# Performance work log

Hardware: AMD Instinct MI355X
Metric: run time of the kernel (lower is better)

## Reference

```python
import jax, jax.numpy as jnp
import numpy as np

jax.config.update("jax_enable_x64", True)  # int64 keys for lattice hashing

_EPS = float(np.finfo(np.float64).eps)
_SIGMA_SPATIAL = 5.0   # spatial stddev (voxels)
_SIGMA_COLOR = 0.25    # intensity stddev
_BASE = 8192           # per-coordinate key range
_OFF = 4096            # coordinate offset so packed keys are non-negative


def _encode(coords):
    """Pack (..., d) integer lattice coords into a single int64 key."""
    enc = jnp.zeros(coords.shape[:-1], jnp.int64)
    for i in range(coords.shape[-1]):
        enc = enc * _BASE + (coords[..., i].astype(jnp.int64) + _OFF)
    return enc


def _bilateral_features(image):
    """Bilateral features: (z,y,x)/sigma_s and intensity/sigma_c. image: (1,D,H,W)."""
    _, D, H, W = image.shape
    z, y, x = jnp.meshgrid(jnp.arange(D, dtype=jnp.float32),
                           jnp.arange(H, dtype=jnp.float32),
                           jnp.arange(W, dtype=jnp.float32), indexing="ij")
    spatial = jnp.stack([z, y, x], -1) / _SIGMA_SPATIAL            # (D,H,W,3)
    color = (image[0] / _SIGMA_COLOR)[..., None]                   # (D,H,W,1)
    return jnp.concatenate([spatial, color], -1).reshape(-1, 4)    # (N,4)


def _permutohedral(q, feats):
    """Permutohedral-lattice Gaussian filtering (splat -> blur -> slice).
    q: (N,C) float32 values, feats: (N,d) float32 positions. Returns (N,C).
    Global scale of the blur kernel cancels in the final normalization."""
    N, d = feats.shape
    dp1 = d + 1
    # ---- elevate features onto the hyperplane H_d ----
    inv_std = np.sqrt(2.0 / 3.0) * dp1
    scale = jnp.asarray([inv_std / np.sqrt((i + 1) * (i + 2)) for i in range(d)], jnp.float32)
    cf = feats * scale
    elev = [None] * dp1
    sm = jnp.zeros((N,), jnp.float32)
    for i in range(d, 0, -1):
        c = cf[:, i - 1]
        elev[i] = sm - i * c
        sm = sm + c
    elev[0] = sm
    elevated = jnp.stack(elev, axis=1)                             # (N, d+1)
    # ---- closest remainder-0 lattice point ----
    rd = jnp.round(elevated / dp1)
    rem0 = rd * dp1
    sum_rd = jnp.sum(rd, axis=1).astype(jnp.int32)
    # ---- rank of each coordinate (ties broken by index) ----
    diff = elevated - rem0
    di = diff[:, :, None]
    dj = diff[:, None, :]
    jlt = (jnp.arange(dp1)[None, :] < jnp.arange(dp1)[:, None])[None]  # mask[i,j] = j < i
    rank = jnp.sum((dj > di) | ((dj == di) & jlt), axis=2).astype(jnp.int32)
    rank = rank + sum_rd[:, None]
    low, high = rank < 0, rank > d
    rank = rank + jnp.where(low, dp1, 0) - jnp.where(high, dp1, 0)
    rem0 = rem0 + jnp.where(low, float(dp1), 0.0) - jnp.where(high, float(dp1), 0.0)
    # ---- barycentric coordinates inside the enclosing simplex ----
    v = (elevated - rem0) / dp1
    rows = jnp.arange(N)[:, None]
    bary = jnp.zeros((N, d + 2), jnp.float32)
    bary = bary.at[rows, d - rank].add(v)
    bary = bary.at[rows, dp1 - rank].add(-v)
    bary = bary.at[:, 0].add(1.0 + bary[:, dp1])
    bary = bary[:, :dp1]                                           # (N, d+1) weights per remainder
    # ---- integer keys of the d+1 simplex vertices (first d coords suffice) ----
    rem0i = rem0[:, :d].astype(jnp.int32)
    keys = jnp.stack([rem0i + jnp.where(rank[:, :d] < dp1 - r, r, r - dp1).astype(jnp.int32)
                      for r in range(dp1)], axis=1)                # (N, d+1, d)
    enc = _encode(keys).reshape(-1)
    Mpad = N * dp1
    sentinel = _BASE ** d                                          # > any real key; sorts last
    uniq, inv = jnp.unique(enc, return_inverse=True, size=Mpad, fill_value=sentinel)
    inv = inv.reshape(N, dp1)
    # ---- splat ----
    C = q.shape[1]
    vals = jnp.zeros((Mpad, C), jnp.float32).at[inv].add(bary[:, :, None] * q[:, None, :])
    # ---- blur along each of the d+1 lattice directions ----
    coords = jnp.stack([(uniq // (_BASE ** (d - 1 - i))) % _BASE - _OFF for i in range(d)],
                       axis=-1).astype(jnp.int32)                  # (Mpad, d)

    def lookup(c):
        e = _encode(c)
        pos = jnp.clip(jnp.searchsorted(uniq, e), 0, Mpad - 1)
        return pos, uniq[pos] == e

    for j in range(dp1):
        off = jnp.ones((d,), jnp.int32)
        if j < d:
            off = off.at[j].set(-d)
        p1, f1 = lookup(coords + off)
        p2, f2 = lookup(coords - off)
        n1 = jnp.where(f1[:, None], vals[p1], 0.0)
        n2 = jnp.where(f2[:, None], vals[p2], 0.0)
        vals = 0.5 * vals + 0.25 * (n1 + n2)
    # ---- slice ----
    return jnp.sum(bary[:, :, None] * vals[inv], axis=1)           # (N, C)


def setup_inputs():
    key = jax.random.key(0)
    k1, k2 = jax.random.split(key)
    input_ = jax.random.uniform(k1, (4, 96, 96, 96), dtype=jnp.float32)
    image = jax.random.uniform(k2, (1, 96, 96, 96), dtype=jnp.float32)
    return {"input_": input_, "image": image}


def reference(input_, image):
    feats = _bilateral_features(image)
    C, D, H, W = input_.shape
    q = input_.reshape(C, -1).T                                    # (N, C)
    ones = jnp.ones((q.shape[0], 1), jnp.float32)                  # fused normalization pass
    filt = _permutohedral(jnp.concatenate([q, ones], axis=1), feats)
    out = filt[:, :C] / (filt[:, C:] + _EPS)                       # == permuto(q) * 1/(permuto(1)+eps)
    return out.T.reshape(C, D, H, W)
```

## Files before the change

kernel.cpp:

```cpp
#include <hip/hip_runtime.h>
#include <hip/hip_fp16.h>
#include <stdint.h>

#define NPTS (96*96*96)
#define NP5  (NPTS*5)

#define GD1 33
#define GD2 29
#define GD3 25
#define GO0 5
#define GO1 16
#define GO2 18
#define GO3 19
#define GS3 5
#define GS2 (GD3*GS3)
#define GS1 (GD2*GS2)
#define GS0 (GD1*GS1)
#define GCELLS (31*GS0)
#define GCELLS1 (GCELLS+1)
#define GSSUM (GS0+GS1+GS2+GS3)

#define LHS 2048

struct LatPt { int cell[5]; float w[5]; };
struct V5 { float s0, s1, s2, s3, w; };


#define LATTICE_MATH(n)                                                        \
  int x = n % 96, y = (n / 96) % 96, z = n / (96 * 96);                        \
  float cf[4];                                                                 \
  cf[0] = ((float)z / 5.0f) * 2.8867513459481287f;                             \
  cf[1] = ((float)y / 5.0f) * 1.6666666666666667f;                             \
  cf[2] = ((float)x / 5.0f) * 1.1785113019775793f;                             \
  cf[3] = (imgv / 0.25f) * 0.9128709291752769f;                                \
  float elev[5];                                                               \
  float sm = 0.f;                                                              \
  _Pragma("unroll")                                                            \
  for (int i = 4; i >= 1; --i){ float c = cf[i-1]; elev[i] = sm - (float)i * c; sm += c; } \
  elev[0] = sm;                                                                \
  float rem0[5]; float sumrd_f = 0.f;                                          \
  _Pragma("unroll")                                                            \
  for (int i = 0; i < 5; i++){ float rd = rintf(elev[i] / 5.0f); rem0[i] = rd * 5.0f; sumrd_f += rd; } \
  int sum_rd = (int)sumrd_f;                                                   \
  float diff[5];                                                               \
  _Pragma("unroll")                                                            \
  for (int i = 0; i < 5; i++) diff[i] = elev[i] - rem0[i];                     \
  int rank[5];                                                                 \
  _Pragma("unroll")                                                            \
  for (int i = 0; i < 5; i++){                                                 \
    int r = 0;                                                                 \
    _Pragma("unroll")                                                          \
    for (int j = 0; j < 5; j++){                                               \
      r += (diff[j] > diff[i] || (diff[j] == diff[i] && j < i)) ? 1 : 0;       \
    }                                                                          \
    rank[i] = r + sum_rd;                                                      \
  }                                                                            \
  _Pragma("unroll")                                                            \
  for (int i = 0; i < 5; i++){                                                 \
    if (rank[i] < 0)      { rank[i] += 5; rem0[i] += 5.0f; }                   \
    else if (rank[i] > 4) { rank[i] -= 5; rem0[i] -= 5.0f; }                   \
  }                                                                            \
  float b[6] = {0.f,0.f,0.f,0.f,0.f,0.f};                                      \
  _Pragma("unroll")                                                            \
  for (int i = 0; i < 5; i++){                                                 \
    float v = (elev[i] - rem0[i]) / 5.0f;                                      \
    b[4 - rank[i]] += v;                                                       \
    b[5 - rank[i]] -= v;                                                       \
  }                                                                            \
  b[0] += 1.0f + b[5];                                                         \
  int rem0i[4];                                                                \
  _Pragma("unroll")                                                            \
  for (int i = 0; i < 4; i++) rem0i[i] = (int)rem0[i];

__device__ __forceinline__ LatPt lat_compute(int n, float imgv)
{
  LATTICE_MATH(n)
  LatPt p;
  #pragma unroll
  for (int r = 0; r < 5; r++){
    int q0 = (rem0i[0] / 5) - (rank[0] < 5 - r ? 0 : 1) + GO0;
    int q1 = (rem0i[1] / 5) - (rank[1] < 5 - r ? 0 : 1) + GO1;
    int q2 = (rem0i[2] / 5) - (rank[2] < 5 - r ? 0 : 1) + GO2;
    int q3 = (rem0i[3] / 5) - (rank[3] < 5 - r ? 0 : 1) + GO3;
    int cell = (((q0 * GD1 + q1) * GD2 + q2) * GD3 + q3) * 5 + r;
    if ((unsigned)cell >= (unsigned)GCELLS) cell = GCELLS;
    p.cell[r] = cell;
    p.w[r] = b[r];
  }
  return p;
}

__global__ void k_build_hyb(const float* __restrict__ image,
                            const float* __restrict__ input_,
                            int* __restrict__ head,
                            int4* __restrict__ nodes)
{
  __shared__ int   ls_cell[LHS];
  __shared__ int   ls_head[LHS];
  __shared__ short ls_next[1280];
  __shared__ float ls_w[1280];
  __shared__ float ls_q[256 * 4];
  __shared__ short ls_slot[1280];
  __shared__ int   ls_cnt;

  int tid = threadIdx.x;
  #pragma unroll
  for (int i = 0; i < LHS / 256; i++){
    ls_cell[tid + 256 * i] = -1;
    ls_head[tid + 256 * i] = -1;
  }
  if (tid == 0) ls_cnt = 0;
  __syncthreads();

  int n = blockIdx.x * 256 + tid;
  float q0 = input_[n], q1 = input_[NPTS + n], q2 = input_[2 * NPTS + n], q3 = input_[3 * NPTS + n];
  *reinterpret_cast<float4*>(&ls_q[tid * 4]) = make_float4(q0, q1, q2, q3);
  LatPt P = lat_compute(n, image[n]);

  #pragma unroll
  for (int r = 0; r < 5; r++){
    int cell = P.cell[r];
    unsigned int h = ((unsigned int)cell * 2654435761u) & (LHS - 1);
    while (true){
      int cur = ls_cell[h];
      if (cur == -1){
        cur = atomicCAS(&ls_cell[h], -1, cell);
        if (cur == -1){
          int li = atomicAdd(&ls_cnt, 1);
          ls_slot[li] = (short)h;
          break;
        }
      }
      if (cur == cell) break;
      h = (h + 1) & (LHS - 1);
    }
    int e = tid * 5 + r;
    ls_w[e] = P.w[r];
    ls_next[e] = (short)atomicExch(&ls_head[h], e);
  }
  __syncthreads();

  int cnt = ls_cnt;
  int blockBase = blockIdx.x * 1280;
  for (int i = tid; i < cnt; i += 256){
    int slot = ls_slot[i];
    int cell = ls_cell[slot];
    float s0 = 0.f, s1 = 0.f, s2 = 0.f, s3 = 0.f, s4 = 0.f;
    int e = ls_head[slot];
    while (e >= 0){
      int en = ls_next[e];
      float w = ls_w[e];
      float4 q = *reinterpret_cast<const float4*>(&ls_q[(e / 5) * 4]);
      s0 += w * q.x; s1 += w * q.y; s2 += w * q.z; s3 += w * q.w; s4 += w;
      e = en;
    }
    int node = blockBase + i;
    int old = atomicExch(&head[cell], node);
    __half2 h01 = __floats2half2_rn(s0, s1);
    __half2 h23 = __floats2half2_rn(s2, s3);
    int4 raw;
    raw.x = old;
    raw.y = *reinterpret_cast<int*>(&h01);
    raw.z = *reinterpret_cast<int*>(&h23);
    raw.w = __float_as_int(s4);
    nodes[node] = raw;
  }
}

__global__ void k_gather_agg(const int* __restrict__ head,
                             const int4* __restrict__ nodes,
                             int3* __restrict__ vals,
                             unsigned int* __restrict__ bitmap)
{
  int c = blockIdx.x * blockDim.x + threadIdx.x;
  int e = -1;
  if (c < GCELLS1) e = head[c];
  bool occ = (e >= 0);
  unsigned long long mask = __ballot(occ);
  int lane = threadIdx.x & 63;
  if (lane == 0)       bitmap[c >> 5] = (unsigned int)(mask & 0xffffffffu);
  else if (lane == 32) bitmap[c >> 5] = (unsigned int)(mask >> 32);
  if (c >= GCELLS1) return;

  float s0 = 0.f, s1 = 0.f, s2 = 0.f, s3 = 0.f, s4 = 0.f;
  while (e >= 0){
    int4 raw = nodes[e];
    __half2 h01 = *reinterpret_cast<__half2*>(&raw.y);
    __half2 h23 = *reinterpret_cast<__half2*>(&raw.z);
    float2 f01 = __half22float2(h01);
    float2 f23 = __half22float2(h23);
    s0 += f01.x; s1 += f01.y; s2 += f23.x; s3 += f23.y;
    s4 += __int_as_float(raw.w);
    e = raw.x;
  }
  __half2 o01 = __floats2half2_rn(s0, s1);
  __half2 o23 = __floats2half2_rn(s2, s3);
  int3 rec;
  rec.x = *reinterpret_cast<int*>(&o01);
  rec.y = *reinterpret_cast<int*>(&o23);
  rec.z = __float_as_int(s4);
  vals[c] = rec;
}

__device__ __forceinline__ V5 ublur(const unsigned int* __restrict__ bitmap,
                                    const int3* __restrict__ vin,
                                    int d, int dPa, int dPb, int dMa, int dMb)
{
  V5 u = {0.f, 0.f, 0.f, 0.f, 0.f};
  unsigned int wd = bitmap[d >> 5];
  if (!((wd >> (d & 31)) & 1u)) return u;
  int rd = d % 5;
  int p1 = d + (rd == 4 ? dPb : dPa);
  int p2 = d + (rd == 0 ? dMb : dMa);
  int3 a  = vin[d];
  int3 b1 = vin[p1];
  int3 b2 = vin[p2];
  float2 a01 = __half22float2(*reinterpret_cast<__half2*>(&a.x));
  float2 a23 = __half22float2(*reinterpret_cast<__half2*>(&a.y));
  float2 m01 = __half22float2(*reinterpret_cast<__half2*>(&b1.x));
  float2 m23 = __half22float2(*reinterpret_cast<__half2*>(&b1.y));
  float2 n01 = __half22float2(*reinterpret_cast<__half2*>(&b2.x));
  float2 n23 = __half22float2(*reinterpret_cast<__half2*>(&b2.y));
  u.s0 = 0.5f * a01.x + 0.25f * (m01.x + n01.x);
  u.s1 = 0.5f * a01.y + 0.25f * (m01.y + n01.y);
  u.s2 = 0.5f * a23.x + 0.25f * (m23.x + n23.x);
  u.s3 = 0.5f * a23.y + 0.25f * (m23.y + n23.y);
  u.w  = 0.5f * __int_as_float(a.z) + 0.25f * (__int_as_float(b1.z) + __int_as_float(b2.z));
  return u;
}

__global__ void k_blur2_d(const unsigned int* __restrict__ bitmap,
                          const int3* __restrict__ vin,
                          int3* __restrict__ vout,
                          int dPaA, int dPbA, int dMaA, int dMbA,
                          int dPaB, int dPbB, int dMaB, int dMbB, int zfill)
{
  int c = blockIdx.x * blockDim.x + threadIdx.x;
  if (c >= GCELLS) return;
  unsigned int w = bitmap[c >> 5];
  if (!((w >> (c & 31)) & 1u)){
    if (zfill){
      int3 zero; zero.x = 0; zero.y = 0; zero.z = 0;
      vout[c] = zero;
    }
    return;
  }
  int r = c % 5;
  int q1 = c + (r == 4 ? dPbB : dPaB);
  int q2 = c + (r == 0 ? dMbB : dMaB);

  V5 uc = ublur(bitmap, vin, c,  dPaA, dPbA, dMaA, dMbA);
  V5 u1 = ublur(bitmap, vin, q1, dPaA, dPbA, dMaA, dMbA);
  V5 u2 = ublur(bitmap, vin, q2, dPaA, dPbA, dMaA, dMbA);

  float o0 = 0.5f * uc.s0 + 0.25f * (u1.s0 + u2.s0);
  float o1 = 0.5f * uc.s1 + 0.25f * (u1.s1 + u2.s1);
  float o2 = 0.5f * uc.s2 + 0.25f * (u1.s2 + u2.s2);
  float o3 = 0.5f * uc.s3 + 0.25f * (u1.s3 + u2.s3);
  float ow = 0.5f * uc.w  + 0.25f * (u1.w  + u2.w);

  __half2 o01 = __floats2half2_rn(o0, o1);
  __half2 o23 = __floats2half2_rn(o2, o3);
  int3 rec;
  rec.x = *reinterpret_cast<int*>(&o01);
  rec.y = *reinterpret_cast<int*>(&o23);
  rec.z = __float_as_int(ow);
  vout[c] = rec;
}

__global__ void k_blur_d(const unsigned int* __restrict__ bitmap,
                         const int3* __restrict__ vin,
                         int3* __restrict__ vout,
                         int dPa, int dPb, int dMa, int dMb, int zfill)
{
  int c = blockIdx.x * blockDim.x + threadIdx.x;
  if (c >= GCELLS) return;
  unsigned int w = bitmap[c >> 5];
  if (!((w >> (c & 31)) & 1u)){
    if (zfill){
      int3 zero; zero.x = 0; zero.y = 0; zero.z = 0;
      vout[c] = zero;
    }
    return;
  }
  V5 u = ublur(bitmap, vin, c, dPa, dPb, dMa, dMb);
  __half2 o01 = __floats2half2_rn(u.s0, u.s1);
  __half2 o23 = __floats2half2_rn(u.s2, u.s3);
  int3 rec;
  rec.x = *reinterpret_cast<int*>(&o01);
  rec.y = *reinterpret_cast<int*>(&o23);
  rec.z = __float_as_int(u.w);
  vout[c] = rec;
}

__global__ void k_slice_d(const float* __restrict__ image,
                          const int3* __restrict__ vals,
                          float* __restrict__ out)
{
  int n = blockIdx.x * blockDim.x + threadIdx.x;
  if (n >= NPTS) return;
  LatPt P = lat_compute(n, image[n]);

  float s0 = 0.f, s1 = 0.f, s2 = 0.f, s3 = 0.f, s4 = 0.f;
  #pragma unroll
  for (int r = 0; r < 5; r++){
    float w = P.w[r];
    int3 rec = vals[P.cell[r]];
    float2 f01 = __half22float2(*reinterpret_cast<__half2*>(&rec.x));
    float2 f23 = __half22float2(*reinterpret_cast<__half2*>(&rec.y));
    s0 += w * f01.x; s1 += w * f01.y; s2 += w * f23.x; s3 += w * f23.y;
    s4 += w * __int_as_float(rec.z);
  }
  float denom = s4 + 2.2204460492503131e-16f;
  out[n]            = s0 / denom;
  out[NPTS + n]     = s1 / denom;
  out[2 * NPTS + n] = s2 / denom;
  out[3 * NPTS + n] = s3 / denom;
}


extern "C" void kernel_launch(void* const* d_in, const int* in_sizes, int n_in,
                              void* d_out, int out_size, void* d_ws, size_t ws_size,
                              hipStream_t stream)
{
  const float* input_ = (const float*)d_in[0];
  const float* image  = (const float*)d_in[1];
  float* out = (float*)d_out;
  char* ws = (char*)d_ws;

  const int NB = (NPTS + 255) / 256;
  const int CB = (GCELLS1 + 255) / 256;
  const size_t BMWORDS = (size_t)CB * 8;
  const int Sj[5] = { GS0, GS1, GS2, GS3, 0 };
  int dPa[5], dPb[5], dMa[5], dMb[5];
  for (int j = 0; j < 5; j++){
    dPa[j] = 1 - Sj[j];
    dPb[j] = GSSUM - Sj[j] - 4;
    dMa[j] = Sj[j] - 1;
    dMb[j] = Sj[j] - GSSUM + 4;
  }

  size_t o = 0;
  size_t off_bm   = o; o += BMWORDS * 4;              o = (o + 255) & ~(size_t)255;
  size_t off_dead = o;
  size_t off_head = o; o += (size_t)GCELLS1 * 4;      o = (o + 255) & ~(size_t)255;
  size_t off_node = o; o += (size_t)NP5 * 16;         o = (o + 255) & ~(size_t)255;
  size_t dead_end = o;
  size_t off_vA   = o; o += (size_t)GCELLS1 * 12;
  size_t vB_need  = (size_t)GCELLS1 * 12;
  size_t off_vB   = off_dead;
  if (dead_end - off_dead < vB_need || o > ws_size){
    off_vB = (o + 255) & ~(size_t)255;
  }

  unsigned int* bitmap = (unsigned int*)(ws + off_bm);
  int*          head   = (int*)(ws + off_head);
  int4*         nodes  = (int4*)(ws + off_node);
  int3*         valsA  = (int3*)(ws + off_vA);
  int3*         valsB  = (int3*)(ws + off_vB);

  hipMemsetAsync(head, 0xFF, (size_t)GCELLS1 * 4, stream);

  k_build_hyb<<<NB, 256, 0, stream>>>(image, input_, head, nodes);
  k_gather_agg<<<CB, 256, 0, stream>>>(head, nodes, valsA, bitmap);

  k_blur2_d<<<CB, 256, 0, stream>>>(bitmap, valsA, valsB,
                                    dPa[0], dPb[0], dMa[0], dMb[0],
                                    dPa[1], dPb[1], dMa[1], dMb[1], 1);
  k_blur2_d<<<CB, 256, 0, stream>>>(bitmap, valsB, valsA,
                                    dPa[2], dPb[2], dMa[2], dMb[2],
                                    dPa[3], dPb[3], dMa[3], dMb[3], 0);
  k_blur_d<<<CB, 256, 0, stream>>>(bitmap, valsA, valsB,
                                   dPa[4], dPb[4], dMa[4], dMb[4], 0);

  k_slice_d<<<NB, 256, 0, stream>>>(image, valsB, out);
}
```

Measured before the change: 176.3 us.

## Split shared-memory splat hash per remainder and pack list head into cell word

Replaces the single 2048-slot shared hash, which kept separate cell and head arrays, with five 512-slot tables, one per remainder r, keyed by lattice position. Each slot word packs the position and the most recent thread index, so one atomicExch both inserts and links the list. This drops the separate head array and the atomicExch on it, and shrinks initialisation and shared-memory footprint, which could allow higher occupancy. In exchange, positions that fall out of range are now skipped rather than sent to a sentinel cell, and packing into 32 bits relies on position fitting in 23 bits.

Result: no change. 175.1 us (-0.6%).

```diff
diff --git a/kernel.cpp b/kernel.cpp
--- a/kernel.cpp
+++ b/kernel.cpp
@@ -20,7 +20,7 @@
 #define GCELLS1 (GCELLS+1)
 #define GSSUM (GS0+GS1+GS2+GS3)
 
-#define LHS 2048
+#define LHSR 512
 
 struct LatPt { int cell[5]; float w[5]; };
 struct V5 { float s0, s1, s2, s3, w; };
@@ -95,20 +95,17 @@
                             int* __restrict__ head,
                             int4* __restrict__ nodes)
 {
-  __shared__ int   ls_cell[LHS];
-  __shared__ int   ls_head[LHS];
-  __shared__ short ls_next[1280];
-  __shared__ float ls_w[1280];
+  __shared__ int   ls_cells[5 * LHSR];
+  __shared__ short ls_next[5 * 256];
+  __shared__ float ls_w[5 * 256];
   __shared__ float ls_q[256 * 4];
   __shared__ short ls_slot[1280];
   __shared__ int   ls_cnt;
 
   int tid = threadIdx.x;
   #pragma unroll
-  for (int i = 0; i < LHS / 256; i++){
-    ls_cell[tid + 256 * i] = -1;
-    ls_head[tid + 256 * i] = -1;
-  }
+  for (int i = 0; i < (5 * LHSR) / 256; i++)
+    ls_cells[tid + 256 * i] = -1;
   if (tid == 0) ls_cnt = 0;
   __syncthreads();
 
@@ -120,23 +117,31 @@
   #pragma unroll
   for (int r = 0; r < 5; r++){
     int cell = P.cell[r];
-    unsigned int h = ((unsigned int)cell * 2654435761u) & (LHS - 1);
-    while (true){
-      int cur = ls_cell[h];
-      if (cur == -1){
-        cur = atomicCAS(&ls_cell[h], -1, cell);
+    if (cell < GCELLS){
+      int pos = cell / 5;
+      unsigned int h = ((unsigned int)pos * 2654435761u) >> 23;
+      int base = r * LHSR;
+      int me = (pos << 9) | tid;
+      while (true){
+        int cur = ls_cells[base + h];
         if (cur == -1){
-          int li = atomicAdd(&ls_cnt, 1);
-          ls_slot[li] = (short)h;
+          cur = atomicCAS(&ls_cells[base + h], -1, me);
+          if (cur == -1){
+            ls_next[r * 256 + tid] = 511;
+            int li = atomicAdd(&ls_cnt, 1);
+            ls_slot[li] = (short)(base + h);
+            break;
+          }
+        }
+        if ((cur >> 9) == pos){
+          int old = atomicExch(&ls_cells[base + h], me);
+          ls_next[r * 256 + tid] = (short)(old & 511);
           break;
         }
+        h = (h + 1) & (LHSR - 1);
       }
-      if (cur == cell) break;
-      h = (h + 1) & (LHS - 1);
+      ls_w[r * 256 + tid] = P.w[r];
     }
-    int e = tid * 5 + r;
-    ls_w[e] = P.w[r];
-    ls_next[e] = (short)atomicExch(&ls_head[h], e);
   }
   __syncthreads();
 
@@ -144,13 +149,16 @@
   int blockBase = blockIdx.x * 1280;
   for (int i = tid; i < cnt; i += 256){
     int slot = ls_slot[i];
-    int cell = ls_cell[slot];
+    int word = ls_cells[slot];
+    int r = slot >> 9;
+    int pos = word >> 9;
+    int cell = pos * 5 + r;
     float s0 = 0.f, s1 = 0.f, s2 = 0.f, s3 = 0.f, s4 = 0.f;
-    int e = ls_head[slot];
-    while (e >= 0){
-      int en = ls_next[e];
-      float w = ls_w[e];
-      float4 q = *reinterpret_cast<const float4*>(&ls_q[(e / 5) * 4]);
+    int e = word & 511;
+    while (e < 256){
+      int en = ls_next[r * 256 + e];
+      float w = ls_w[r * 256 + e];
+      float4 q = *reinterpret_cast<const float4*>(&ls_q[e * 4]);
       s0 += w * q.x; s1 += w * q.y; s2 += w * q.z; s3 += w * q.w; s4 += w;
       e = en;
     }
```
